# Performance work log

Hardware: AMD Instinct MI355X
Metric: run time of the kernel (lower is better)

## Reference

```python
import jax, jax.numpy as jnp
import numpy as np


def gcn_conv(x, W, b, src, dst, num_nodes):
    # PyG GCNConv: h = D^{-1/2} (A + I) D^{-1/2} (x W) + b
    h = x @ W  # [N, H]
    ones = jnp.ones(src.shape[0], dtype=h.dtype)
    deg = jax.ops.segment_sum(ones, dst, num_segments=num_nodes) + 1.0  # +1 for self-loop
    d_inv_sqrt = jax.lax.rsqrt(deg)
    norm = d_inv_sqrt[src] * d_inv_sqrt[dst]  # [E]
    msg = h[src] * norm[:, None]  # [E, H] gather
    agg = jax.ops.segment_sum(msg, dst, num_segments=num_nodes)  # scatter-add
    agg = agg + h * (1.0 / deg)[:, None]  # self-loop term: deg_i^{-1/2} * deg_i^{-1/2}
    return agg + b


def setup_inputs() -> dict:
    key = jax.random.key(0)
    ks = jax.random.split(key, 10)
    N, E, F, H, C, G = 100000, 1000000, 64, 128, 2, 512
    x = jax.random.normal(ks[0], (N, F), dtype=jnp.float32)
    edge_index = jax.random.randint(ks[1], (2, E), 0, N, dtype=jnp.int64)
    batch = jnp.sort(jax.random.randint(ks[2], (N,), 0, G, dtype=jnp.int64))
    s1 = 1.0 / np.sqrt(F)
    s2 = 1.0 / np.sqrt(H)
    W1 = jax.random.normal(ks[3], (F, H), dtype=jnp.float32) * s1
    b1 = jnp.zeros((H,), dtype=jnp.float32)
    W2 = jax.random.normal(ks[4], (H, H), dtype=jnp.float32) * s2
    b2 = jnp.zeros((H,), dtype=jnp.float32)
    Wfc = jax.random.normal(ks[5], (H, C), dtype=jnp.float32) * s2
    bfc = jnp.zeros((C,), dtype=jnp.float32)
    return {"x": x, "edge_index": edge_index, "batch": batch, "num_graphs": G,
            "W1": W1, "b1": b1, "W2": W2, "b2": b2, "Wfc": Wfc, "bfc": bfc}


def reference(x, edge_index, batch, num_graphs, W1, b1, W2, b2, Wfc, bfc):
    # Dropout is inference-mode (identity), matching model.eval().
    N = x.shape[0]
    src, dst = edge_index[0], edge_index[1]
    h = gcn_conv(x, W1, b1, src, dst, N)
    h = jax.nn.relu(h)
    h = gcn_conv(h, W2, b2, src, dst, N)
    h = jax.nn.relu(h)
    # global mean pool over graphs
    summed = jax.ops.segment_sum(h, batch, num_segments=num_graphs)  # [G, H]
    counts = jax.ops.segment_sum(jnp.ones((N,), h.dtype), batch, num_segments=num_graphs)
    pooled = summed / jnp.maximum(counts, 1.0)[:, None]
    logits = pooled @ Wfc + bfc  # [G, C]
    return jax.nn.softmax(logits, axis=1)
```

## Files before the change

### kernel.cpp

```cpp
#include <hip/hip_runtime.h>
#include <hip/hip_bf16.h>

typedef __hip_bfloat16 bf16;
typedef __attribute__((ext_vector_type(8))) short short8;
typedef __attribute__((ext_vector_type(4))) float f32x4;
typedef __attribute__((ext_vector_type(2))) float f32x2;

#define FDIM 64
#define HDIM 128

#define ESTRIDE 4096
#define EC 8192
#define ECPT (EC / 256)

__device__ __forceinline__ float b2f(bf16 v) { return __bfloat162float(v); }
__device__ __forceinline__ float bits2f(unsigned int u) {
    return __uint_as_float(u << 16);
}
__device__ __forceinline__ unsigned short f2bits(float f) {
    bf16 b = __float2bfloat16(f);
    return *reinterpret_cast<unsigned short*>(&b);
}
__device__ __forceinline__ unsigned char f2fp8(float v) {
    int pk = __builtin_amdgcn_cvt_pk_fp8_f32(v, v, 0, false);
    return (unsigned char)(pk & 0xFF);
}

__device__ __forceinline__ int edge_word(const int* e, long long logical_idx, int is64) {
    return is64 ? e[2 * logical_idx] : e[logical_idx];
}

__global__ __launch_bounds__(256) void k_phase1(const int* __restrict__ edge,
                                                int* __restrict__ gcur,
                                                int* __restrict__ ebuf,
                                                int E,
                                                const void* __restrict__ W1, const void* __restrict__ b1,
                                                const void* __restrict__ W2, const void* __restrict__ b2,
                                                const void* __restrict__ Wfc, const void* __restrict__ bfc,
                                                bf16* __restrict__ W1t, bf16* __restrict__ W2t,
                                                bf16* __restrict__ b1c, bf16* __restrict__ b2c,
                                                bf16* __restrict__ Wfcc, bf16* __restrict__ bfcc,
                                                const void* __restrict__ x,
                                                unsigned char* __restrict__ X8,
                                                int totalX4,
                                                int* __restrict__ flags,
                                                const int* __restrict__ batch,
                                                int* __restrict__ gstart,
                                                int N, int G,
                                                int NB1, int WB, int XB) {
    int blk = blockIdx.x;
    int tid = threadIdx.x;
    if (blk < NB1) {
        unsigned long long zb = __ballot(edge[2 * (tid & 63) + 1] == 0);
        int is64 = (__popcll(zb) > 32);
        __shared__ int h[512];
        for (int b2 = tid; b2 < 512; b2 += 256) h[b2] = 0;
        __syncthreads();
        int e0 = blk * EC;
        int dcache[ECPT];
#pragma unroll
        for (int k = 0; k < ECPT; k++) {
            int i = e0 + (k << 8) + tid;
            int d = -1;
            if (i < E) d = edge_word(edge, (long long)E + i, is64);
            dcache[k] = d;
            if (d >= 0) atomicAdd(&h[(d >> 8) & 511], 1);
        }
        __syncthreads();
        for (int b2 = tid; b2 < 512; b2 += 256) {
            int c = h[b2];
            h[b2] = c ? atomicAdd(&gcur[b2], c) : 0;
        }
        __syncthreads();
#pragma unroll
        for (int k = 0; k < ECPT; k++) {
            int i = e0 + (k << 8) + tid;
            int d = dcache[k];
            if (d >= 0) {
                int s = edge_word(edge, i, is64);
                int bb = (d >> 8) & 511;
                int pos = atomicAdd(&h[bb], 1);
                if ((unsigned)pos < (unsigned)ESTRIDE)
                    ebuf[(bb << 12) + pos] = s | ((d & 255) << 24);
            }
        }
    } else if (blk < NB1 + WB) {
        const unsigned short* w1u = (const unsigned short*)W1;
        unsigned short wv = w1u[2 * (tid & 63)];
        int ee = (wv >> 7) & 0xFF;
        unsigned long long wb2 = __ballot(ee == 0 || ee >= 137);
        int f0 = (__popcll(wb2) > 4);
        if (blk == NB1 && tid == 0) flags[0] = f0;
        int gid = (blk - NB1) * 256 + tid;
        int stride = WB * 256;
#define CV(src, si) (f0 ? __float2bfloat16(((const float*)(src))[si]) : ((const bf16*)(src))[si])
        for (int i = gid; i < FDIM * HDIM; i += stride) {
            int n = i >> 6, k = i & 63;
            W1t[i] = CV(W1, k * HDIM + n);
        }
        for (int i = gid; i < HDIM * HDIM; i += stride) {
            int n = i >> 7, k = i & 127;
            W2t[i] = CV(W2, k * HDIM + n);
        }
        for (int i = gid; i < HDIM; i += stride) b1c[i] = CV(b1, i);
        for (int i = gid; i < HDIM; i += stride) b2c[i] = CV(b2, i);
        for (int i = gid; i < HDIM * 2; i += stride) Wfcc[i] = CV(Wfc, i);
        for (int i = gid; i < 2; i += stride) bfcc[i] = CV(bfc, i);
#undef CV
    } else if (blk < NB1 + WB + XB) {
        const unsigned short* w1u = (const unsigned short*)W1;
        unsigned short wv = w1u[2 * (tid & 63)];
        int ee = (wv >> 7) & 0xFF;
        unsigned long long wb2 = __ballot(ee == 0 || ee >= 137);
        int f0 = (__popcll(wb2) > 4);
        int t = (blk - NB1 - WB) * 256 + tid;
        if (t >= totalX4) return;
        float4 v;
        if (f0) {
            v = ((const float4*)x)[t];
        } else {
            uint2 p = ((const uint2*)x)[t];
            v.x = bits2f(p.x & 0xFFFFu); v.y = bits2f(p.x >> 16);
            v.z = bits2f(p.y & 0xFFFFu); v.w = bits2f(p.y >> 16);
        }
        unsigned int q0 = (unsigned int)__builtin_amdgcn_cvt_pk_fp8_f32(v.x, v.y, 0, false) & 0xFFFFu;
        unsigned int q1 = (unsigned int)__builtin_amdgcn_cvt_pk_fp8_f32(v.z, v.w, 0, false) & 0xFFFFu;
        ((unsigned int*)X8)[t] = (q1 << 16) | q0;
    } else {
        int bv = batch[1025 + 2 * (tid & 63)];
        unsigned long long bb2 = __ballot(bv == 0);
        int is64 = (__popcll(bb2) > 32);
        int i = (blk - NB1 - WB - XB) * 256 + tid;
        if (i >= N) return;
        int bi = is64 ? batch[2 * i] : batch[i];
        if (i == 0) {
            for (int g = 0; g <= bi; g++) gstart[g] = 0;
        } else {
            int bp = is64 ? batch[2 * (i - 1)] : batch[i - 1];
            for (int g = bp + 1; g <= bi; g++) gstart[g] = i;
        }
        if (i == N - 1) {
            for (int g = bi + 1; g <= G; g++) gstart[g] = N;
        }
    }
}

__global__ __launch_bounds__(256) void k_csr(const int* __restrict__ ebuf,
                                             const int* __restrict__ gcur,
                                             int* __restrict__ rowptr,
                                             int* __restrict__ cnt,
                                             float* __restrict__ dinv,
                                             int* __restrict__ srclist,
                                             int N) {
    __shared__ int sred[256];
    __shared__ int sc[256];
    __shared__ int sa[256], sb[256];
    int b = blockIdx.x;
    int tid = threadIdx.x;
    int part = 0;
    for (int j = tid; j < b; j += 256) {
        int v = gcur[j];
        part += (v > ESTRIDE) ? ESTRIDE : v;
    }
    sred[tid] = part;
    __syncthreads();
    for (int s = 128; s > 0; s >>= 1) {
        if (tid < s) sred[tid] += sred[tid + s];
        __syncthreads();
    }
    int gbase = sred[0];
    int cnt_b = gcur[b];
    if (cnt_b > ESTRIDE) cnt_b = ESTRIDE;
    sc[tid] = 0;
    __syncthreads();
    const int* eb = ebuf + (b << 12);
    for (int j = tid; j < cnt_b; j += 256) {
        int p = eb[j];
        atomicAdd(&sc[(unsigned)p >> 24], 1);
    }
    __syncthreads();
    int cval = sc[tid];
    sa[tid] = cval;
    __syncthreads();
    int* cur = sa; int* nxt = sb;
    for (int off = 1; off < 256; off <<= 1) {
        int v = cur[tid];
        if (tid >= off) v += cur[tid - off];
        nxt[tid] = v;
        __syncthreads();
        int* t = cur; cur = nxt; nxt = t;
    }
    int excl = cur[tid] - cval;
    int node = (b << 8) + tid;
    if (node < N) {
        rowptr[node] = gbase + excl;
        cnt[node] = cval;
        dinv[node] = rsqrtf((float)cval + 1.0f);
    }
    __syncthreads();
    sc[tid] = excl;
    __syncthreads();
    for (int j = tid; j < cnt_b; j += 256) {
        int p = eb[j];
        int pos = atomicAdd(&sc[(unsigned)p >> 24], 1);
        srclist[gbase + pos] = p & 0xFFFFFF;
    }
}

#define ACC4(w, e, o) do { \
    f32x2 fA = __builtin_amdgcn_cvt_pk_f32_fp8((w), false); \
    f32x2 fB = __builtin_amdgcn_cvt_pk_f32_fp8((w), true); \
    acc[(o)+0] += fA[0] * (e); acc[(o)+1] += fA[1] * (e); \
    acc[(o)+2] += fB[0] * (e); acc[(o)+3] += fB[1] * (e); } while (0)
#define ACC16(u4, e) do { ACC4((u4).x, (e), 0); ACC4((u4).y, (e), 4); \
                          ACC4((u4).z, (e), 8); ACC4((u4).w, (e), 12); } while (0)

__device__ __forceinline__ uint4 packbf16x8(const float* a) {
    uint4 p;
    p.x = ((unsigned int)f2bits(a[1]) << 16) | f2bits(a[0]);
    p.y = ((unsigned int)f2bits(a[3]) << 16) | f2bits(a[2]);
    p.z = ((unsigned int)f2bits(a[5]) << 16) | f2bits(a[4]);
    p.w = ((unsigned int)f2bits(a[7]) << 16) | f2bits(a[6]);
    return p;
}

__global__ __launch_bounds__(256) void k_agg64(const unsigned char* __restrict__ x8,
                                               const int* __restrict__ srclist,
                                               const int* __restrict__ rowptr,
                                               const int* __restrict__ count,
                                               const float* __restrict__ dinv,
                                               bf16* __restrict__ outb, int N) {
    int wave = threadIdx.x >> 6;
    int lane = threadIdx.x & 63;
    int group = lane >> 2;
    int sub = lane & 3;
    int i = blockIdx.x * 64 + wave * 16 + group;
    if (i >= N) return;
    int start = rowptr[i];
    int cnt = count[i];
    float di = dinv[i];
    const uint4* hrow = (const uint4*)x8;
    float acc[16];
#pragma unroll
    for (int k = 0; k < 16; k++) acc[k] = 0.f;
    int lb = group << 2;
    for (int jb = 0; jb < cnt; jb += 4) {
        int m = cnt - jb; if (m > 4) m = 4;
        int sv = srclist[start + jb + ((sub < m) ? sub : (m - 1))];
        float dvv = dinv[sv];
        if (m == 4) {
            int s[4]; float e[4]; uint4 v[4];
#pragma unroll
            for (int t = 0; t < 4; t++) { s[t] = __shfl(sv, lb + t); e[t] = __shfl(dvv, lb + t); }
#pragma unroll
            for (int t = 0; t < 4; t++) v[t] = hrow[(size_t)s[t] * 4 + sub];
#pragma unroll
            for (int t = 0; t < 4; t++) ACC16(v[t], e[t]);
        } else {
            for (int j = 0; j < m; j++) {
                int s0 = __shfl(sv, lb + j); float e0 = __shfl(dvv, lb + j);
                uint4 v0 = hrow[(size_t)s0 * 4 + sub];
                ACC16(v0, e0);
            }
        }
    }
    {
        uint4 vs = hrow[(size_t)i * 4 + sub];
        float self = di * di;
        float sacc[16];
#pragma unroll
        for (int k = 0; k < 16; k++) sacc[k] = 0.f;
        {
            float* acc = sacc;
            ACC16(vs, self);
        }
#pragma unroll
        for (int k = 0; k < 16; k++) acc[k] = di * acc[k] + sacc[k];
    }
    uint4 p0 = packbf16x8(&acc[0]);
    uint4 p1 = packbf16x8(&acc[8]);
    ((uint4*)outb)[(size_t)i * 8 + sub * 2 + 0] = p0;
    ((uint4*)outb)[(size_t)i * 8 + sub * 2 + 1] = p1;
}

__global__ __launch_bounds__(256) void k_agg128(const unsigned char* __restrict__ h8,
                                                const int* __restrict__ srclist,
                                                const int* __restrict__ rowptr,
                                                const int* __restrict__ count,
                                                const float* __restrict__ dinv,
                                                bf16* __restrict__ outb, int N) {
    int wave = threadIdx.x >> 6;
    int lane = threadIdx.x & 63;
    int group = lane >> 3;
    int sub = lane & 7;
    int i = blockIdx.x * 32 + wave * 8 + group;
    if (i >= N) return;
    int start = rowptr[i];
    int cnt = count[i];
    float di = dinv[i];
    const uint4* hrow = (const uint4*)h8;
    float acc[16];
#pragma unroll
    for (int k = 0; k < 16; k++) acc[k] = 0.f;
    int lb = group << 3;
    for (int jb = 0; jb < cnt; jb += 8) {
        int m = cnt - jb; if (m > 8) m = 8;
        int sv = srclist[start + jb + ((sub < m) ? sub : (m - 1))];
        float dvv = dinv[sv];
        if (m == 8) {
            int s[8]; float e[8]; uint4 v[8];
#pragma unroll
            for (int t = 0; t < 8; t++) { s[t] = __shfl(sv, lb + t); e[t] = __shfl(dvv, lb + t); }
#pragma unroll
            for (int t = 0; t < 8; t++) v[t] = hrow[(size_t)s[t] * 8 + sub];
#pragma unroll
            for (int t = 0; t < 8; t++) ACC16(v[t], e[t]);
        } else {
            int j = 0;
            for (; j + 4 <= m; j += 4) {
                int s0 = __shfl(sv, lb + j + 0); float e0 = __shfl(dvv, lb + j + 0);
                int s1 = __shfl(sv, lb + j + 1); float e1 = __shfl(dvv, lb + j + 1);
                int s2 = __shfl(sv, lb + j + 2); float e2 = __shfl(dvv, lb + j + 2);
                int s3 = __shfl(sv, lb + j + 3); float e3 = __shfl(dvv, lb + j + 3);
                uint4 v0 = hrow[(size_t)s0 * 8 + sub];
                uint4 v1 = hrow[(size_t)s1 * 8 + sub];
                uint4 v2 = hrow[(size_t)s2 * 8 + sub];
                uint4 v3 = hrow[(size_t)s3 * 8 + sub];
                ACC16(v0, e0); ACC16(v1, e1); ACC16(v2, e2); ACC16(v3, e3);
            }
            for (; j < m; j++) {
                int s0 = __shfl(sv, lb + j); float e0 = __shfl(dvv, lb + j);
                uint4 v0 = hrow[(size_t)s0 * 8 + sub];
                ACC16(v0, e0);
            }
        }
    }
    {
        uint4 vs = hrow[(size_t)i * 8 + sub];
        float self = di * di;
        float sacc[16];
#pragma unroll
        for (int k = 0; k < 16; k++) sacc[k] = 0.f;
        {
            float* acc = sacc;
            ACC16(vs, self);
        }
#pragma unroll
        for (int k = 0; k < 16; k++) acc[k] = di * acc[k] + sacc[k];
    }
    uint4 p0 = packbf16x8(&acc[0]);
    uint4 p1 = packbf16x8(&acc[8]);
    ((uint4*)outb)[(size_t)i * 16 + sub * 2 + 0] = p0;
    ((uint4*)outb)[(size_t)i * 16 + sub * 2 + 1] = p1;
}

#define K1PAD 72
__global__ __launch_bounds__(256) void k_gemmA(const bf16* __restrict__ Y,
                                               const bf16* __restrict__ W1t,
                                               const bf16* __restrict__ bias,
                                               unsigned char* __restrict__ h8, int N) {
    __shared__ bf16 As[64 * K1PAD];
    __shared__ bf16 Wt[HDIM * K1PAD];
    __shared__ float bsf[HDIM];
    int tid = threadIdx.x;
    int base = blockIdx.x * 64;
    {
        const uint4* wsrc = (const uint4*)W1t;
        for (int i = tid; i < HDIM * 8; i += 256) {
            int n = i >> 3, c = i & 7;
            *(uint4*)&Wt[n * K1PAD + c * 8] = wsrc[n * 8 + c];
        }
    }
    {
        const uint4* xb = (const uint4*)Y;
        for (int i = tid; i < 64 * 8; i += 256) {
            int r = i >> 3, c = i & 7;
            int gr = base + r; if (gr >= N) gr = N - 1;
            *(uint4*)&As[r * K1PAD + c * 8] = xb[(size_t)gr * 8 + c];
        }
    }
    if (tid < HDIM) bsf[tid] = b2f(bias[tid]);
    __syncthreads();
    int wid = tid >> 6, lane = tid & 63;
    int l15 = lane & 15, q = lane >> 4;
    int m0 = wid * 16;
    short8 af[2];
#pragma unroll
    for (int kc = 0; kc < 2; kc++)
        af[kc] = *(const short8*)&As[(m0 + l15) * K1PAD + kc * 32 + q * 8];
    f32x4 acc[8];
#pragma unroll
    for (int nt = 0; nt < 8; nt++) {
        acc[nt] = (f32x4){0.f, 0.f, 0.f, 0.f};
#pragma unroll
        for (int kc = 0; kc < 2; kc++) {
            short8 bf = *(const short8*)&Wt[(nt * 16 + l15) * K1PAD + kc * 32 + q * 8];
            acc[nt] = __builtin_amdgcn_mfma_f32_16x16x32_bf16(af[kc], bf, acc[nt], 0, 0, 0);
        }
    }
#pragma unroll
    for (int nt = 0; nt < 8; nt++) {
        int col = nt * 16 + l15;
        float bv = bsf[col];
#pragma unroll
        for (int r = 0; r < 4; r++) {
            int gr = base + m0 + q * 4 + r;
            if (gr < N) {
                float v = fmaxf(acc[nt][r] + bv, 0.f);
                h8[(size_t)gr * HDIM + col] = f2fp8(v);
            }
        }
    }
}

#define K2PAD 136
__global__ __launch_bounds__(256) void k_gemmB(const bf16* __restrict__ Z,
                                               const bf16* __restrict__ W2t,
                                               const bf16* __restrict__ bias,
                                               bf16* __restrict__ outp, int N) {
    __shared__ bf16 As[64 * K2PAD];
    __shared__ bf16 Wt[HDIM * K2PAD];
    __shared__ float bsf[HDIM];
    int tid = threadIdx.x;
    int base = blockIdx.x * 64;
    {
        const uint4* wsrc = (const uint4*)W2t;
        for (int i = tid; i < HDIM * 16; i += 256) {
            int n = i >> 4, c = i & 15;
            *(uint4*)&Wt[n * K2PAD + c * 8] = wsrc[n * 16 + c];
        }
    }
    const uint4* xb = (const uint4*)Z;
    for (int i = tid; i < 64 * 16; i += 256) {
        int r = i >> 4, c = i & 15;
        int gr = base + r; if (gr >= N) gr = N - 1;
        *(uint4*)&As[r * K2PAD + c * 8] = xb[(size_t)gr * 16 + c];
    }
    if (tid < HDIM) bsf[tid] = b2f(bias[tid]);
    __syncthreads();
    int wid = tid >> 6, lane = tid & 63;
    int l15 = lane & 15, q = lane >> 4;
    int m0 = wid * 16;
    short8 af[4];
#pragma unroll
    for (int kc = 0; kc < 4; kc++)
        af[kc] = *(const short8*)&As[(m0 + l15) * K2PAD + kc * 32 + q * 8];
    f32x4 acc[8];
#pragma unroll
    for (int nt = 0; nt < 8; nt++) {
        acc[nt] = (f32x4){0.f, 0.f, 0.f, 0.f};
#pragma unroll
        for (int kc = 0; kc < 4; kc++) {
            short8 bf = *(const short8*)&Wt[(nt * 16 + l15) * K2PAD + kc * 32 + q * 8];
            acc[nt] = __builtin_amdgcn_mfma_f32_16x16x32_bf16(af[kc], bf, acc[nt], 0, 0, 0);
        }
    }
#pragma unroll
    for (int nt = 0; nt < 8; nt++) {
        int col = nt * 16 + l15;
        float bv = bsf[col];
#pragma unroll
        for (int r = 0; r < 4; r++) {
            int gr = base + m0 + q * 4 + r;
            if (gr < N) outp[(size_t)gr * HDIM + col] = __float2bfloat16(fmaxf(acc[nt][r] + bv, 0.f));
        }
    }
}

__global__ __launch_bounds__(256) void k_pool(const bf16* __restrict__ hact,
                                              const int* __restrict__ gstart,
                                              const bf16* __restrict__ Wfc,
                                              const bf16* __restrict__ bfc,
                                              void* __restrict__ out,
                                              const int* __restrict__ flags) {
    __shared__ float lds[16][HDIM + 1];
    __shared__ float colsum[HDIM];
    int g = blockIdx.x;
    int s = gstart[g], e = gstart[g + 1];
    int tid = threadIdx.x;
    int cslot = tid & 15;
    int rslot = tid >> 4;
    const uint4* hp = (const uint4*)hact;
    float a[8] = {0.f, 0.f, 0.f, 0.f, 0.f, 0.f, 0.f, 0.f};
    for (int r = s + rslot; r < e; r += 16) {
        uint4 v = hp[(size_t)r * 16 + cslot];
        a[0] += bits2f(v.x & 0xFFFFu); a[1] += bits2f(v.x >> 16);
        a[2] += bits2f(v.y & 0xFFFFu); a[3] += bits2f(v.y >> 16);
        a[4] += bits2f(v.z & 0xFFFFu); a[5] += bits2f(v.z >> 16);
        a[6] += bits2f(v.w & 0xFFFFu); a[7] += bits2f(v.w >> 16);
    }
#pragma unroll
    for (int k = 0; k < 8; k++) lds[rslot][cslot * 8 + k] = a[k];
    __syncthreads();
    if (tid < HDIM) {
        float sum = 0.f;
#pragma unroll
        for (int k = 0; k < 16; k++) sum += lds[k][tid];
        colsum[tid] = sum;
    }
    __syncthreads();
    if (tid >= 64) return;
    int lane = tid;
    float inv = 1.0f / fmaxf((float)(e - s), 1.0f);
    float m0 = colsum[2 * lane] * inv;
    float m1 = colsum[2 * lane + 1] * inv;
    float l0 = m0 * b2f(Wfc[(2 * lane) * 2 + 0]) + m1 * b2f(Wfc[(2 * lane + 1) * 2 + 0]);
    float l1 = m0 * b2f(Wfc[(2 * lane) * 2 + 1]) + m1 * b2f(Wfc[(2 * lane + 1) * 2 + 1]);
    for (int sft = 32; sft; sft >>= 1) { l0 += __shfl_down(l0, sft); l1 += __shfl_down(l1, sft); }
    if (lane == 0) {
        float z0 = l0 + b2f(bfc[0]);
        float z1 = l1 + b2f(bfc[1]);
        float mx = fmaxf(z0, z1);
        float e0 = expf(z0 - mx), e1 = expf(z1 - mx);
        float sm = e0 + e1;
        float p0 = e0 / sm, p1 = e1 / sm;
        if (flags[0]) {
            ((float*)out)[2 * g + 0] = p0;
            ((float*)out)[2 * g + 1] = p1;
        } else {
            ((bf16*)out)[2 * g + 0] = __float2bfloat16(p0);
            ((bf16*)out)[2 * g + 1] = __float2bfloat16(p1);
        }
    }
}

extern "C" void kernel_launch(void* const* d_in, const int* in_sizes, int n_in,
                              void* d_out, int out_size, void* d_ws, size_t ws_size,
                              hipStream_t stream) {
    const void* x    = d_in[0];
    const int*  edge = (const int*)d_in[1];
    const int*  batch= (const int*)d_in[2];
    const void* W1  = d_in[4];
    const void* b1  = d_in[5];
    const void* W2  = d_in[6];
    const void* b2  = d_in[7];
    const void* Wfc = d_in[8];
    const void* bfc = d_in[9];

    int N = in_sizes[0] / FDIM;
    int E = in_sizes[1] / 2;
    int G = out_size / 2;

    int*   flags  = (int*)d_ws;
    float* dinv   = (float*)((char*)d_ws + 64);
    int*   gcur   = (int*)(dinv + N);
    int*   gstart = gcur + 512;
    int*   rowptr = gstart + 516;
    int*   count  = rowptr + N;
    int*   srclist= count + N;
    int*   ebuf   = srclist + E;
    bf16*  Abuf   = (bf16*)(ebuf + 512 * ESTRIDE);
    bf16*  Bbuf   = Abuf + (size_t)N * HDIM;
    bf16*  b1c    = Bbuf + (size_t)N * HDIM;
    bf16*  b2c    = b1c + HDIM;
    bf16*  Wfcc   = b2c + HDIM;
    bf16*  bfcc   = Wfcc + 256;
    bf16*  W1t    = bfcc + 64;
    bf16*  W2t    = W1t + FDIM * HDIM;
    unsigned char* H8 = (unsigned char*)(W2t + HDIM * HDIM);
    unsigned char* X8 = H8 + (size_t)N * HDIM;

    bf16* Y = Abuf;
    bf16* Z = Abuf;

    int NB  = (N + 255) >> 8;
    int NB1 = (E + EC - 1) / EC;
    int WB = 32;
    int XB = (N * 16 + 255) / 256;
    int BB = (N + 255) / 256;
    int totalX4 = N * 16;

    hipMemsetAsync(gcur, 0, 512 * sizeof(int), stream);
    k_phase1<<<NB1 + WB + XB + BB, 256, 0, stream>>>(edge, gcur, ebuf, E,
                                                     W1, b1, W2, b2, Wfc, bfc,
                                                     W1t, W2t, b1c, b2c, Wfcc, bfcc,
                                                     x, X8, totalX4, flags,
                                                     batch, gstart, N, G,
                                                     NB1, WB, XB);
    k_csr<<<NB, 256, 0, stream>>>(ebuf, gcur, rowptr, count, dinv, srclist, N);

    k_agg64<<<(N + 63) / 64, 256, 0, stream>>>(X8, srclist, rowptr, count, dinv, Y, N);
    k_gemmA<<<(N + 63) / 64, 256, 0, stream>>>(Y, W1t, b1c, H8, N);

    k_agg128<<<(N + 31) / 32, 256, 0, stream>>>(H8, srclist, rowptr, count, dinv, Z, N);
    k_gemmB<<<(N + 63) / 64, 256, 0, stream>>>(Z, W2t, b2c, Bbuf, N);

    k_pool<<<G, 256, 0, stream>>>(Bbuf, gstart, Wfcc, bfcc, d_out, flags);
}
```

Measured before the change: 230.7 us.

## Restructure neighbor aggregation into padded 8-edge chunks with dual-chunk load batching

```diff
diff --git a/kernel.cpp b/kernel.cpp
--- a/kernel.cpp
+++ b/kernel.cpp
@@ -207,6 +207,16 @@
     }
 }
 
+#define ACC8(u2, e) do { \
+    f32x2 f01 = __builtin_amdgcn_cvt_pk_f32_fp8((u2).x, false); \
+    f32x2 f23 = __builtin_amdgcn_cvt_pk_f32_fp8((u2).x, true); \
+    f32x2 f45 = __builtin_amdgcn_cvt_pk_f32_fp8((u2).y, false); \
+    f32x2 f67 = __builtin_amdgcn_cvt_pk_f32_fp8((u2).y, true); \
+    acc[0] += f01[0] * (e); acc[1] += f01[1] * (e); \
+    acc[2] += f23[0] * (e); acc[3] += f23[1] * (e); \
+    acc[4] += f45[0] * (e); acc[5] += f45[1] * (e); \
+    acc[6] += f67[0] * (e); acc[7] += f67[1] * (e); } while (0)
+
 #define ACC4(w, e, o) do { \
     f32x2 fA = __builtin_amdgcn_cvt_pk_f32_fp8((w), false); \
     f32x2 fB = __builtin_amdgcn_cvt_pk_f32_fp8((w), true); \
@@ -223,6 +233,17 @@
     p.w = ((unsigned int)f2bits(a[7]) << 16) | f2bits(a[6]);
     return p;
 }
+
+#define LDCH(V, EV, c_, ROWW) do { \
+    int jb_ = (c_) << 3; int mm_ = cnt - jb_; if (mm_ > 8) mm_ = 8; \
+    int svl_ = srclist[start + jb_ + ((sub < mm_) ? sub : (mm_ - 1))]; \
+    float dvl_ = dinv[svl_]; \
+    _Pragma("unroll") \
+    for (int t_ = 0; t_ < 8; t_++) { \
+        int st_ = __shfl(svl_, lb + t_); float et_ = __shfl(dvl_, lb + t_); \
+        EV[t_] = (t_ < mm_) ? et_ : 0.f; \
+        V[t_] = hrow[(size_t)st_ * (ROWW) + sub]; \
+    } } while (0)
 
 __global__ __launch_bounds__(256) void k_agg64(const unsigned char* __restrict__ x8,
                                                const int* __restrict__ srclist,
@@ -232,55 +253,44 @@
                                                bf16* __restrict__ outb, int N) {
     int wave = threadIdx.x >> 6;
     int lane = threadIdx.x & 63;
-    int group = lane >> 2;
-    int sub = lane & 3;
-    int i = blockIdx.x * 64 + wave * 16 + group;
+    int group = lane >> 3;
+    int sub = lane & 7;
+    int i = blockIdx.x * 32 + wave * 8 + group;
     if (i >= N) return;
     int start = rowptr[i];
     int cnt = count[i];
     float di = dinv[i];
-    const uint4* hrow = (const uint4*)x8;
-    float acc[16];
-#pragma unroll
-    for (int k = 0; k < 16; k++) acc[k] = 0.f;
-    int lb = group << 2;
-    for (int jb = 0; jb < cnt; jb += 4) {
-        int m = cnt - jb; if (m > 4) m = 4;
-        int sv = srclist[start + jb + ((sub < m) ? sub : (m - 1))];
-        float dvv = dinv[sv];
-        if (m == 4) {
-            int s[4]; float e[4]; uint4 v[4];
-#pragma unroll
-            for (int t = 0; t < 4; t++) { s[t] = __shfl(sv, lb + t); e[t] = __shfl(dvv, lb + t); }
-#pragma unroll
-            for (int t = 0; t < 4; t++) v[t] = hrow[(size_t)s[t] * 4 + sub];
-#pragma unroll
-            for (int t = 0; t < 4; t++) ACC16(v[t], e[t]);
-        } else {
-            for (int j = 0; j < m; j++) {
-                int s0 = __shfl(sv, lb + j); float e0 = __shfl(dvv, lb + j);
-                uint4 v0 = hrow[(size_t)s0 * 4 + sub];
-                ACC16(v0, e0);
-            }
+    const uint2* hrow = (const uint2*)x8;
+    float acc[8] = {0.f, 0.f, 0.f, 0.f, 0.f, 0.f, 0.f, 0.f};
+    int lb = group << 3;
+    int nch = (cnt + 7) >> 3;
+    uint2 vA[8], vB[8]; float eA[8], eB[8];
+    if (nch == 2) {
+        LDCH(vA, eA, 0, 8); LDCH(vB, eB, 1, 8);
+#pragma unroll
+        for (int t = 0; t < 8; t++) ACC8(vA[t], eA[t]);
+#pragma unroll
+        for (int t = 0; t < 8; t++) ACC8(vB[t], eB[t]);
+    } else {
+        for (int c = 0; c < nch; c++) {
+            LDCH(vA, eA, c, 8);
+#pragma unroll
+            for (int t = 0; t < 8; t++) ACC8(vA[t], eA[t]);
         }
     }
     {
-        uint4 vs = hrow[(size_t)i * 4 + sub];
+        uint2 vs = hrow[(size_t)i * 8 + sub];
         float self = di * di;
-        float sacc[16];
-#pragma unroll
-        for (int k = 0; k < 16; k++) sacc[k] = 0.f;
+        float sacc[8] = {0.f, 0.f, 0.f, 0.f, 0.f, 0.f, 0.f, 0.f};
         {
             float* acc = sacc;
-            ACC16(vs, self);
-        }
-#pragma unroll
-        for (int k = 0; k < 16; k++) acc[k] = di * acc[k] + sacc[k];
-    }
-    uint4 p0 = packbf16x8(&acc[0]);
-    uint4 p1 = packbf16x8(&acc[8]);
-    ((uint4*)outb)[(size_t)i * 8 + sub * 2 + 0] = p0;
-    ((uint4*)outb)[(size_t)i * 8 + sub * 2 + 1] = p1;
+            ACC8(vs, self);
+        }
+#pragma unroll
+        for (int k = 0; k < 8; k++) acc[k] = di * acc[k] + sacc[k];
+    }
+    uint4 pv = packbf16x8(acc);
+    ((uint4*)outb)[(size_t)i * 8 + sub] = pv;
 }
 
 __global__ __launch_bounds__(256) void k_agg128(const unsigned char* __restrict__ h8,
@@ -303,36 +313,19 @@
 #pragma unroll
     for (int k = 0; k < 16; k++) acc[k] = 0.f;
     int lb = group << 3;
-    for (int jb = 0; jb < cnt; jb += 8) {
-        int m = cnt - jb; if (m > 8) m = 8;
-        int sv = srclist[start + jb + ((sub < m) ? sub : (m - 1))];
-        float dvv = dinv[sv];
-        if (m == 8) {
-            int s[8]; float e[8]; uint4 v[8];
-#pragma unroll
-            for (int t = 0; t < 8; t++) { s[t] = __shfl(sv, lb + t); e[t] = __shfl(dvv, lb + t); }
-#pragma unroll
-            for (int t = 0; t < 8; t++) v[t] = hrow[(size_t)s[t] * 8 + sub];
-#pragma unroll
-            for (int t = 0; t < 8; t++) ACC16(v[t], e[t]);
-        } else {
-            int j = 0;
-            for (; j + 4 <= m; j += 4) {
-                int s0 = __shfl(sv, lb + j + 0); float e0 = __shfl(dvv, lb + j + 0);
-                int s1 = __shfl(sv, lb + j + 1); float e1 = __shfl(dvv, lb + j + 1);
-                int s2 = __shfl(sv, lb + j + 2); float e2 = __shfl(dvv, lb + j + 2);
-                int s3 = __shfl(sv, lb + j + 3); float e3 = __shfl(dvv, lb + j + 3);
-                uint4 v0 = hrow[(size_t)s0 * 8 + sub];
-                uint4 v1 = hrow[(size_t)s1 * 8 + sub];
-                uint4 v2 = hrow[(size_t)s2 * 8 + sub];
-                uint4 v3 = hrow[(size_t)s3 * 8 + sub];
-                ACC16(v0, e0); ACC16(v1, e1); ACC16(v2, e2); ACC16(v3, e3);
-            }
-            for (; j < m; j++) {
-                int s0 = __shfl(sv, lb + j); float e0 = __shfl(dvv, lb + j);
-                uint4 v0 = hrow[(size_t)s0 * 8 + sub];
-                ACC16(v0, e0);
-            }
+    int nch = (cnt + 7) >> 3;
+    uint4 vA[8], vB[8]; float eA[8], eB[8];
+    if (nch == 2) {
+        LDCH(vA, eA, 0, 8); LDCH(vB, eB, 1, 8);
+#pragma unroll
+        for (int t = 0; t < 8; t++) ACC16(vA[t], eA[t]);
+#pragma unroll
+        for (int t = 0; t < 8; t++) ACC16(vB[t], eB[t]);
+    } else {
+        for (int c = 0; c < nch; c++) {
+            LDCH(vA, eA, c, 8);
+#pragma unroll
+            for (int t = 0; t < 8; t++) ACC16(vA[t], eA[t]);
         }
     }
     {
@@ -579,7 +572,7 @@
                                                      NB1, WB, XB);
     k_csr<<<NB, 256, 0, stream>>>(ebuf, gcur, rowptr, count, dinv, srclist, N);
 
-    k_agg64<<<(N + 63) / 64, 256, 0, stream>>>(X8, srclist, rowptr, count, dinv, Y, N);
+    k_agg64<<<(N + 31) / 32, 256, 0, stream>>>(X8, srclist, rowptr, count, dinv, Y, N);
     k_gemmA<<<(N + 63) / 64, 256, 0, stream>>>(Y, W1t, b1c, H8, N);
 
     k_agg128<<<(N + 31) / 32, 256, 0, stream>>>(H8, srclist, rowptr, count, dinv, Z, N);
```

Result: faster. 225.9 us (-2.0%).
